# Kernel tuning notes

Measured on AMD Instinct MI355X. Metric: run time of the kernel, lower is better.

## Reference

```python
import jax, jax.numpy as jnp
import numpy as np

E = 16        # ensemble size
D_IN = 512    # input_dim
H = 512       # hidden width (hidden=[512,512])
D_OUT = 1     # output_dim
B = 8192      # batch


def _xavier(key, shape, fan_in, fan_out):
    # Xavier/Glorot uniform, matching layer_init='Xavier'
    limit = np.sqrt(6.0 / (fan_in + fan_out)).astype(np.float32)
    return jax.random.uniform(key, shape, jnp.float32, -limit, limit)


def setup_inputs() -> dict:
    key = jax.random.key(0)
    ks = jax.random.split(key, 7)
    x = jax.random.normal(ks[0], (B, D_IN), dtype=jnp.float32)
    # stacked per-ensemble-member weights (equivalent to E independent MLPs)
    W1 = _xavier(ks[1], (E, D_IN, H), D_IN, H)
    b1 = jnp.zeros((E, H), dtype=jnp.float32)
    W2 = _xavier(ks[2], (E, H, H), H, H)
    b2 = jnp.zeros((E, H), dtype=jnp.float32)
    W3 = _xavier(ks[3], (E, H, D_OUT), H, D_OUT)
    b3 = jnp.zeros((E, D_OUT), dtype=jnp.float32)
    return {"x": x, "W1": W1, "b1": b1, "W2": W2, "b2": b2, "W3": W3, "b3": b3}


def reference(x, W1, b1, W2, b2, W3, b3):
    # Batched over the ensemble dim: one grouped GEMM per layer instead of E small ones.
    h1 = jax.nn.relu(jnp.einsum('bi,eih->ebh', x, W1) + b1[:, None, :])   # [E,B,H]
    h2 = jax.nn.relu(jnp.einsum('ebh,ehk->ebk', h1, W2) + b2[:, None, :])  # [E,B,H]
    out = jnp.einsum('ebh,eho->ebo', h2, W3) + b3[:, None, :]              # [E,B,D_OUT]
    return out
```

## Files before the change

kernel.cpp:

```cpp
#include <hip/hip_runtime.h>


#define E_N   16
#define DIN   512
#define HID   512
#define BATCH 8192
#define BT    64
#define NBT   (BATCH / BT)
#define NBLK  (E_N * NBT)

typedef __attribute__((ext_vector_type(8))) short bf16x8;
typedef __attribute__((ext_vector_type(4))) float f32x4;

#define IMG_BYTES   131072
#define XPACK_BYTES ((size_t)NBT * IMG_BYTES)
#define WP_PER_E    (32 * 16 * 2048)
#define WP_BYTES    ((size_t)E_N * WP_PER_E)

__device__ __forceinline__ short f2bf(float f) {
  unsigned u = __builtin_bit_cast(unsigned, f);
  u += 0x7fffu + ((u >> 16) & 1u);
  return (short)(u >> 16);
}
__device__ __forceinline__ float bf2f(short s) {
  unsigned u = ((unsigned)(unsigned short)s) << 16;
  return __builtin_bit_cast(float, u);
}

__global__ void pack_x_kernel(const float* __restrict__ x, char* __restrict__ xp) {
  int t  = blockIdx.x * blockDim.x + threadIdx.x;
  int b  = t >> 6;
  int c8 = (t & 63) << 3;
  const float* src = x + (size_t)b * DIN + c8;
  bf16x8 hi, lo;
#pragma unroll
  for (int j = 0; j < 8; ++j) {
    float v = src[j];
    short h = f2bf(v);
    hi[j] = h;
    lo[j] = f2bf(v - bf2f(h));
  }
  int btile = b >> 6, r = b & 63;
  char* img = xp + (size_t)btile * IMG_BYTES;
  int inrow = (c8 << 1) ^ ((r & 7) << 4);
  *(bf16x8*)(img + (r << 10) + inrow) = hi;
  *(bf16x8*)(img + 65536 + (r << 10) + inrow) = lo;
}

__global__ void pack_w_kernel(const float* __restrict__ w, char* __restrict__ wp) {
  int t    = blockIdx.x * blockDim.x + threadIdx.x;
  int lane = t & 63;
  int kb   = (t >> 6) & 15;
  int nt   = (t >> 10) & 31;
  int e    = t >> 15;
  int k0 = kb * 32 + (lane >> 4) * 8;
  int n  = nt * 16 + (lane & 15);
  const float* src = w + ((size_t)e * DIN + k0) * HID + n;
  bf16x8 hi, lo;
#pragma unroll
  for (int j = 0; j < 8; ++j) {
    float v = src[(size_t)j * HID];
    short h = f2bf(v);
    hi[j] = h;
    lo[j] = f2bf(v - bf2f(h));
  }
  char* dst = wp + ((size_t)((e * 32 + nt) * 16 + kb) << 11) + (lane << 4);
  *(bf16x8*)dst = hi;
  *(bf16x8*)(dst + 1024) = lo;
}

#define MFMA(A, B, C) __builtin_amdgcn_mfma_f32_16x16x32_bf16(A, B, C, 0, 0, 0)

__global__ __launch_bounds__(512, 2) void fused_mlp_kernel(
    const char* __restrict__ xp,
    const char* __restrict__ wp1,
    const char* __restrict__ wp2,
    const float* __restrict__ b1,
    const float* __restrict__ b2,
    const float* __restrict__ w3,
    const float* __restrict__ b3,
    float* __restrict__ out)
{
  __shared__ __align__(16) char lds[IMG_BYTES];
  __shared__ float out_acc[BT];

  const int tid  = threadIdx.x;
  const int lane = tid & 63;
  const int wid  = tid >> 6;

  const int bid   = blockIdx.x;
  const int xcd   = bid & 7;
  const int slot  = bid >> 3;
  const int e     = (xcd << 1) | (slot >> 7);
  const int btile = slot & 127;

  {
    const char* src = xp + (size_t)btile * IMG_BYTES;
#pragma unroll
    for (int it = 0; it < 16; ++it) {
      int off = (it << 13) + (tid << 4);
      *(bf16x8*)(lds + off) = *(const bf16x8*)(src + off);
    }
  }
  if (tid < BT) out_acc[tid] = b3[e];

  const int swzA = (lane & 7) << 4;
  const int h4   = (lane >> 4) << 4;
  int rb[4];
#pragma unroll
  for (int mt = 0; mt < 4; ++mt) rb[mt] = (mt * 16 + (lane & 15)) << 10;

  float bias1[4], bias2[4], w3v[4];
#pragma unroll
  for (int ntl = 0; ntl < 4; ++ntl) {
    int c = wid * 64 + ntl * 16 + (lane & 15);
    bias1[ntl] = b1[e * HID + c];
    bias2[ntl] = b2[e * HID + c];
    w3v[ntl]   = w3[e * HID + c];
  }

  const char* wpe1 = wp1 + (size_t)e * WP_PER_E + (size_t)wid * (4 * 16 * 2048);
  const char* wpe2 = wp2 + (size_t)e * WP_PER_E + (size_t)wid * (4 * 16 * 2048);

  __syncthreads();

  f32x4 acc[4][4];
#pragma unroll
  for (int mt = 0; mt < 4; ++mt)
#pragma unroll
    for (int ntl = 0; ntl < 4; ++ntl)
      acc[mt][ntl] = (f32x4){0.f, 0.f, 0.f, 0.f};

#pragma unroll 4
  for (int kb = 0; kb < 16; ++kb) {
    bf16x8 Ah[4], Al[4], Bh[4], Bl[4];
    const int ca = ((kb << 6) | h4) ^ swzA;
#pragma unroll
    for (int mt = 0; mt < 4; ++mt) {
      Ah[mt] = *(const bf16x8*)(lds + rb[mt] + ca);
      Al[mt] = *(const bf16x8*)(lds + 65536 + rb[mt] + ca);
    }
#pragma unroll
    for (int ntl = 0; ntl < 4; ++ntl) {
      const char* p = wpe1 + ((ntl * 16 + kb) << 11) + (lane << 4);
      Bh[ntl] = *(const bf16x8*)p;
      Bl[ntl] = *(const bf16x8*)(p + 1024);
    }
#pragma unroll
    for (int mt = 0; mt < 4; ++mt)
#pragma unroll
      for (int ntl = 0; ntl < 4; ++ntl) {
        acc[mt][ntl] = MFMA(Ah[mt], Bh[ntl], acc[mt][ntl]);
        acc[mt][ntl] = MFMA(Ah[mt], Bl[ntl], acc[mt][ntl]);
        acc[mt][ntl] = MFMA(Al[mt], Bh[ntl], acc[mt][ntl]);
      }
  }

  __syncthreads();

#pragma unroll
  for (int mt = 0; mt < 4; ++mt)
#pragma unroll
    for (int ntl = 0; ntl < 4; ++ntl) {
      const int C2 = (wid * 64 + ntl * 16 + (lane & 15)) << 1;
#pragma unroll
      for (int q = 0; q < 4; ++q) {
        const int R = mt * 16 + (lane >> 4) * 4 + q;
        float v = acc[mt][ntl][q] + bias1[ntl];
        v = fmaxf(v, 0.f);
        short hb = f2bf(v);
        short lb = f2bf(v - bf2f(hb));
        const int inrow = C2 ^ ((R & 7) << 4);
        *(short*)(lds + (R << 10) + inrow) = hb;
        *(short*)(lds + 65536 + (R << 10) + inrow) = lb;
      }
    }

  __syncthreads();

#pragma unroll
  for (int mt = 0; mt < 4; ++mt)
#pragma unroll
    for (int ntl = 0; ntl < 4; ++ntl)
      acc[mt][ntl] = (f32x4){0.f, 0.f, 0.f, 0.f};

#pragma unroll 4
  for (int kb = 0; kb < 16; ++kb) {
    bf16x8 Ah[4], Al[4], Bh[4], Bl[4];
    const int ca = ((kb << 6) | h4) ^ swzA;
#pragma unroll
    for (int mt = 0; mt < 4; ++mt) {
      Ah[mt] = *(const bf16x8*)(lds + rb[mt] + ca);
      Al[mt] = *(const bf16x8*)(lds + 65536 + rb[mt] + ca);
    }
#pragma unroll
    for (int ntl = 0; ntl < 4; ++ntl) {
      const char* p = wpe2 + ((ntl * 16 + kb) << 11) + (lane << 4);
      Bh[ntl] = *(const bf16x8*)p;
      Bl[ntl] = *(const bf16x8*)(p + 1024);
    }
#pragma unroll
    for (int mt = 0; mt < 4; ++mt)
#pragma unroll
      for (int ntl = 0; ntl < 4; ++ntl) {
        acc[mt][ntl] = MFMA(Ah[mt], Bh[ntl], acc[mt][ntl]);
        acc[mt][ntl] = MFMA(Ah[mt], Bl[ntl], acc[mt][ntl]);
        acc[mt][ntl] = MFMA(Al[mt], Bh[ntl], acc[mt][ntl]);
      }
  }

#pragma unroll
  for (int mt = 0; mt < 4; ++mt)
#pragma unroll
    for (int q = 0; q < 4; ++q) {
      float p = 0.f;
#pragma unroll
      for (int ntl = 0; ntl < 4; ++ntl)
        p += fmaxf(acc[mt][ntl][q] + bias2[ntl], 0.f) * w3v[ntl];
      p += __shfl_xor(p, 1);
      p += __shfl_xor(p, 2);
      p += __shfl_xor(p, 4);
      p += __shfl_xor(p, 8);
      if ((lane & 15) == 0)
        atomicAdd(&out_acc[mt * 16 + (lane >> 4) * 4 + q], p);
    }

  __syncthreads();
  if (tid < BT)
    out[(size_t)e * BATCH + btile * BT + tid] = out_acc[tid];
}

extern "C" void kernel_launch(void* const* d_in, const int* in_sizes, int n_in,
                              void* d_out, int out_size, void* d_ws, size_t ws_size,
                              hipStream_t stream) {
  (void)in_sizes; (void)n_in; (void)out_size; (void)ws_size;
  const float* x  = (const float*)d_in[0];
  const float* W1 = (const float*)d_in[1];
  const float* b1 = (const float*)d_in[2];
  const float* W2 = (const float*)d_in[3];
  const float* b2 = (const float*)d_in[4];
  const float* W3 = (const float*)d_in[5];
  const float* b3 = (const float*)d_in[6];

  char* xp  = (char*)d_ws;
  char* wp1 = xp + XPACK_BYTES;
  char* wp2 = wp1 + WP_BYTES;

  pack_x_kernel<<<2048, 256, 0, stream>>>(x, xp);
  pack_w_kernel<<<2048, 256, 0, stream>>>(W1, wp1);
  pack_w_kernel<<<2048, 256, 0, stream>>>(W2, wp2);
  fused_mlp_kernel<<<NBLK, 512, 0, stream>>>(xp, wp1, wp2, b1, b2, W3, b3,
                                             (float*)d_out);
}
```

Measured before the change: 438.3 us.

## Switch GEMMs to 32x32x16 MFMA with repacked weights and prefetched B fragments

Replaces the 16x16x32 bf16 MFMA tiling with 32x32x16 MFMA tiles (2x2 per wave), and repacks the weights and the x image with a 16-row XOR swizzle to match the new fragment layout. B fragments for the next k-block are double-buffered in registers so the global loads overlap the current MFMAs. The larger MFMA shape is meant to lower LDS A-fragment reads per flop and raise matrix-core efficiency. In exchange, register pressure rises from the prefetch buffers and 16-wide accumulators, which could hurt occupancy at the 2-blocks launch bound.

After: 492.8 us. 12.4% more time.

```diff
diff --git a/kernel.cpp b/kernel.cpp
--- a/kernel.cpp
+++ b/kernel.cpp
@@ -10,11 +10,11 @@
 #define NBLK  (E_N * NBT)
 
 typedef __attribute__((ext_vector_type(8))) short bf16x8;
-typedef __attribute__((ext_vector_type(4))) float f32x4;
+typedef __attribute__((ext_vector_type(16))) float f32x16;
 
 #define IMG_BYTES   131072
 #define XPACK_BYTES ((size_t)NBT * IMG_BYTES)
-#define WP_PER_E    (32 * 16 * 2048)
+#define WP_PER_E    (1 << 20)
 #define WP_BYTES    ((size_t)E_N * WP_PER_E)
 
 __device__ __forceinline__ short f2bf(float f) {
@@ -42,7 +42,7 @@
   }
   int btile = b >> 6, r = b & 63;
   char* img = xp + (size_t)btile * IMG_BYTES;
-  int inrow = (c8 << 1) ^ ((r & 7) << 4);
+  int inrow = (c8 << 1) ^ ((r & 15) << 4);
   *(bf16x8*)(img + (r << 10) + inrow) = hi;
   *(bf16x8*)(img + 65536 + (r << 10) + inrow) = lo;
 }
@@ -50,11 +50,12 @@
 __global__ void pack_w_kernel(const float* __restrict__ w, char* __restrict__ wp) {
   int t    = blockIdx.x * blockDim.x + threadIdx.x;
   int lane = t & 63;
-  int kb   = (t >> 6) & 15;
-  int nt   = (t >> 10) & 31;
+  int kk   = (t >> 6) & 1;
+  int kb   = (t >> 7) & 15;
+  int nt   = (t >> 11) & 15;
   int e    = t >> 15;
-  int k0 = kb * 32 + (lane >> 4) * 8;
-  int n  = nt * 16 + (lane & 15);
+  int k0 = kb * 32 + kk * 16 + (lane >> 5) * 8;
+  int n  = nt * 32 + (lane & 31);
   const float* src = w + ((size_t)e * DIN + k0) * HID + n;
   bf16x8 hi, lo;
 #pragma unroll
@@ -64,12 +65,24 @@
     hi[j] = h;
     lo[j] = f2bf(v - bf2f(h));
   }
-  char* dst = wp + ((size_t)((e * 32 + nt) * 16 + kb) << 11) + (lane << 4);
+  char* dst = wp + (((size_t)(e * 16 + nt) * 16 + kb) << 12) + (kk << 11) + (lane << 4);
   *(bf16x8*)dst = hi;
   *(bf16x8*)(dst + 1024) = lo;
 }
 
-#define MFMA(A, B, C) __builtin_amdgcn_mfma_f32_16x16x32_bf16(A, B, C, 0, 0, 0)
+#define MFMA32(A, B, C) __builtin_amdgcn_mfma_f32_32x32x16_bf16(A, B, C, 0, 0, 0)
+
+#define LOADB(dst, kb_) do {                                          \
+    const int _k = (kb_) << 12;                                       \
+    dst[0] = *(const bf16x8*)(w0 + _k);                               \
+    dst[1] = *(const bf16x8*)(w0 + _k + 1024);                        \
+    dst[2] = *(const bf16x8*)(w0 + _k + 2048);                        \
+    dst[3] = *(const bf16x8*)(w0 + _k + 3072);                        \
+    dst[4] = *(const bf16x8*)(w1 + _k);                               \
+    dst[5] = *(const bf16x8*)(w1 + _k + 1024);                        \
+    dst[6] = *(const bf16x8*)(w1 + _k + 2048);                        \
+    dst[7] = *(const bf16x8*)(w1 + _k + 3072);                        \
+  } while (0)
 
 __global__ __launch_bounds__(512, 2) void fused_mlp_kernel(
     const char* __restrict__ xp,
@@ -84,9 +97,12 @@
   __shared__ __align__(16) char lds[IMG_BYTES];
   __shared__ float out_acc[BT];
 
-  const int tid  = threadIdx.x;
-  const int lane = tid & 63;
-  const int wid  = tid >> 6;
+  const int tid    = threadIdx.x;
+  const int lane   = tid & 63;
+  const int wid    = tid >> 6;
+  const int lane31 = lane & 31;
+  const int hk16   = (lane >> 5) << 4;
+  const int aswz   = (lane & 15) << 4;
 
   const int bid   = blockIdx.x;
   const int xcd   = bid & 7;
@@ -104,73 +120,81 @@
   }
   if (tid < BT) out_acc[tid] = b3[e];
 
-  const int swzA = (lane & 7) << 4;
-  const int h4   = (lane >> 4) << 4;
-  int rb[4];
-#pragma unroll
-  for (int mt = 0; mt < 4; ++mt) rb[mt] = (mt * 16 + (lane & 15)) << 10;
-
-  float bias1[4], bias2[4], w3v[4];
-#pragma unroll
-  for (int ntl = 0; ntl < 4; ++ntl) {
-    int c = wid * 64 + ntl * 16 + (lane & 15);
+  int arow[2];
+#pragma unroll
+  for (int mt = 0; mt < 2; ++mt) arow[mt] = ((mt << 5) + lane31) << 10;
+
+  float bias1[2], bias2[2], w3v[2];
+#pragma unroll
+  for (int ntl = 0; ntl < 2; ++ntl) {
+    int c = wid * 64 + ntl * 32 + lane31;
     bias1[ntl] = b1[e * HID + c];
     bias2[ntl] = b2[e * HID + c];
     w3v[ntl]   = w3[e * HID + c];
   }
 
-  const char* wpe1 = wp1 + (size_t)e * WP_PER_E + (size_t)wid * (4 * 16 * 2048);
-  const char* wpe2 = wp2 + (size_t)e * WP_PER_E + (size_t)wid * (4 * 16 * 2048);
-
-  __syncthreads();
-
-  f32x4 acc[4][4];
-#pragma unroll
-  for (int mt = 0; mt < 4; ++mt)
-#pragma unroll
-    for (int ntl = 0; ntl < 4; ++ntl)
-      acc[mt][ntl] = (f32x4){0.f, 0.f, 0.f, 0.f};
-
-#pragma unroll 4
-  for (int kb = 0; kb < 16; ++kb) {
-    bf16x8 Ah[4], Al[4], Bh[4], Bl[4];
-    const int ca = ((kb << 6) | h4) ^ swzA;
-#pragma unroll
-    for (int mt = 0; mt < 4; ++mt) {
-      Ah[mt] = *(const bf16x8*)(lds + rb[mt] + ca);
-      Al[mt] = *(const bf16x8*)(lds + 65536 + rb[mt] + ca);
-    }
-#pragma unroll
-    for (int ntl = 0; ntl < 4; ++ntl) {
-      const char* p = wpe1 + ((ntl * 16 + kb) << 11) + (lane << 4);
-      Bh[ntl] = *(const bf16x8*)p;
-      Bl[ntl] = *(const bf16x8*)(p + 1024);
-    }
-#pragma unroll
-    for (int mt = 0; mt < 4; ++mt)
-#pragma unroll
-      for (int ntl = 0; ntl < 4; ++ntl) {
-        acc[mt][ntl] = MFMA(Ah[mt], Bh[ntl], acc[mt][ntl]);
-        acc[mt][ntl] = MFMA(Ah[mt], Bl[ntl], acc[mt][ntl]);
-        acc[mt][ntl] = MFMA(Al[mt], Bh[ntl], acc[mt][ntl]);
-      }
-  }
-
-  __syncthreads();
-
-#pragma unroll
-  for (int mt = 0; mt < 4; ++mt)
-#pragma unroll
-    for (int ntl = 0; ntl < 4; ++ntl) {
-      const int C2 = (wid * 64 + ntl * 16 + (lane & 15)) << 1;
-#pragma unroll
-      for (int q = 0; q < 4; ++q) {
-        const int R = mt * 16 + (lane >> 4) * 4 + q;
-        float v = acc[mt][ntl][q] + bias1[ntl];
+  const char* wA0 = wp1 + (size_t)e * WP_PER_E + ((size_t)(wid * 2 + 0) << 16) + (lane << 4);
+  const char* wA1 = wp1 + (size_t)e * WP_PER_E + ((size_t)(wid * 2 + 1) << 16) + (lane << 4);
+  const char* wB0 = wp2 + (size_t)e * WP_PER_E + ((size_t)(wid * 2 + 0) << 16) + (lane << 4);
+  const char* wB1 = wp2 + (size_t)e * WP_PER_E + ((size_t)(wid * 2 + 1) << 16) + (lane << 4);
+
+  __syncthreads();
+
+  f32x16 acc[2][2];
+
+  auto run_layer = [&](const char* w0, const char* w1) {
+    bf16x8 Bb[2][8];
+    LOADB(Bb[0], 0);
+#pragma unroll
+    for (int kb = 0; kb < 16; ++kb) {
+      if (kb < 15) LOADB(Bb[(kb + 1) & 1], kb + 1);
+      bf16x8 Ah[2][2], Al[2][2];
+#pragma unroll
+      for (int mt = 0; mt < 2; ++mt)
+#pragma unroll
+        for (int kk = 0; kk < 2; ++kk) {
+          const int off = ((kb << 6) + (kk << 5) + hk16) ^ aswz;
+          const char* pa = lds + arow[mt] + off;
+          Ah[mt][kk] = *(const bf16x8*)pa;
+          Al[mt][kk] = *(const bf16x8*)(pa + 65536);
+        }
+#pragma unroll
+      for (int mt = 0; mt < 2; ++mt)
+#pragma unroll
+        for (int ntl = 0; ntl < 2; ++ntl)
+#pragma unroll
+          for (int kk = 0; kk < 2; ++kk) {
+            const int fb = ntl * 4 + kk * 2;
+            acc[mt][ntl] = MFMA32(Ah[mt][kk], Bb[kb & 1][fb],     acc[mt][ntl]);
+            acc[mt][ntl] = MFMA32(Ah[mt][kk], Bb[kb & 1][fb + 1], acc[mt][ntl]);
+            acc[mt][ntl] = MFMA32(Al[mt][kk], Bb[kb & 1][fb],     acc[mt][ntl]);
+          }
+    }
+  };
+
+#pragma unroll
+  for (int mt = 0; mt < 2; ++mt)
+#pragma unroll
+    for (int ntl = 0; ntl < 2; ++ntl)
+      acc[mt][ntl] = (f32x16)(0.f);
+
+  run_layer(wA0, wA1);
+
+  __syncthreads();
+
+#pragma unroll
+  for (int mt = 0; mt < 2; ++mt)
+#pragma unroll
+    for (int ntl = 0; ntl < 2; ++ntl) {
+      const int C2 = (wid * 64 + ntl * 32 + lane31) << 1;
+#pragma unroll
+      for (int reg = 0; reg < 16; ++reg) {
+        const int R = mt * 32 + (reg & 3) + 8 * (reg >> 2) + ((lane >> 5) << 2);
+        float v = acc[mt][ntl][reg] + bias1[ntl];
         v = fmaxf(v, 0.f);
         short hb = f2bf(v);
         short lb = f2bf(v - bf2f(hb));
-        const int inrow = C2 ^ ((R & 7) << 4);
+        const int inrow = C2 ^ ((R & 15) << 4);
         *(short*)(lds + (R << 10) + inrow) = hb;
         *(short*)(lds + 65536 + (R << 10) + inrow) = lb;
       }
@@ -179,50 +203,30 @@
   __syncthreads();
 
 #pragma unroll
-  for (int mt = 0; mt < 4; ++mt)
-#pragma unroll
-    for (int ntl = 0; ntl < 4; ++ntl)
-      acc[mt][ntl] = (f32x4){0.f, 0.f, 0.f, 0.f};
-
-#pragma unroll 4
-  for (int kb = 0; kb < 16; ++kb) {
-    bf16x8 Ah[4], Al[4], Bh[4], Bl[4];
-    const int ca = ((kb << 6) | h4) ^ swzA;
-#pragma unroll
-    for (int mt = 0; mt < 4; ++mt) {
-      Ah[mt] = *(const bf16x8*)(lds + rb[mt] + ca);
-      Al[mt] = *(const bf16x8*)(lds + 65536 + rb[mt] + ca);
-    }
-#pragma unroll
-    for (int ntl = 0; ntl < 4; ++ntl) {
-      const char* p = wpe2 + ((ntl * 16 + kb) << 11) + (lane << 4);
-      Bh[ntl] = *(const bf16x8*)p;
-      Bl[ntl] = *(const bf16x8*)(p + 1024);
-    }
-#pragma unroll
-    for (int mt = 0; mt < 4; ++mt)
-#pragma unroll
-      for (int ntl = 0; ntl < 4; ++ntl) {
-        acc[mt][ntl] = MFMA(Ah[mt], Bh[ntl], acc[mt][ntl]);
-        acc[mt][ntl] = MFMA(Ah[mt], Bl[ntl], acc[mt][ntl]);
-        acc[mt][ntl] = MFMA(Al[mt], Bh[ntl], acc[mt][ntl]);
-      }
-  }
-
-#pragma unroll
-  for (int mt = 0; mt < 4; ++mt)
-#pragma unroll
-    for (int q = 0; q < 4; ++q) {
+  for (int mt = 0; mt < 2; ++mt)
+#pragma unroll
+    for (int ntl = 0; ntl < 2; ++ntl)
+      acc[mt][ntl] = (f32x16)(0.f);
+
+  run_layer(wB0, wB1);
+
+#pragma unroll
+  for (int mt = 0; mt < 2; ++mt)
+#pragma unroll
+    for (int reg = 0; reg < 16; ++reg) {
       float p = 0.f;
 #pragma unroll
-      for (int ntl = 0; ntl < 4; ++ntl)
-        p += fmaxf(acc[mt][ntl][q] + bias2[ntl], 0.f) * w3v[ntl];
+      for (int ntl = 0; ntl < 2; ++ntl)
+        p += fmaxf(acc[mt][ntl][reg] + bias2[ntl], 0.f) * w3v[ntl];
       p += __shfl_xor(p, 1);
       p += __shfl_xor(p, 2);
       p += __shfl_xor(p, 4);
       p += __shfl_xor(p, 8);
-      if ((lane & 15) == 0)
-        atomicAdd(&out_acc[mt * 16 + (lane >> 4) * 4 + q], p);
+      p += __shfl_xor(p, 16);
+      if (lane31 == 0) {
+        const int R = mt * 32 + (reg & 3) + 8 * (reg >> 2) + ((lane >> 5) << 2);
+        atomicAdd(&out_acc[R], p);
+      }
     }
 
   __syncthreads();
```

## Split fused MLP across 16 waves with prefetched B fragments and wider swizzle

Applied to the files above, without the earlier changes.

Doubles the block to 1024 threads so each of 16 waves computes a 64x32 output slice instead of 64x64, raising wave-level parallelism per CU. Weight fragments are software double-buffered across k-steps to hide global load latency behind MFMAs. The LDS XOR swizzle is widened from 8 to 16 rows in both the pack and epilogue writes to cut bank conflicts. In exchange, A fragments are re-read from LDS twice as often per MFMA, and the aggressive launch bounds may constrain registers and cause spills.

Measured after the change: 480.4 us. 9.6% more time.

```diff
diff --git a/kernel.cpp b/kernel.cpp
--- a/kernel.cpp
+++ b/kernel.cpp
@@ -42,7 +42,7 @@
   }
   int btile = b >> 6, r = b & 63;
   char* img = xp + (size_t)btile * IMG_BYTES;
-  int inrow = (c8 << 1) ^ ((r & 7) << 4);
+  int inrow = (c8 << 1) ^ ((r & 15) << 4);
   *(bf16x8*)(img + (r << 10) + inrow) = hi;
   *(bf16x8*)(img + 65536 + (r << 10) + inrow) = lo;
 }
@@ -69,9 +69,17 @@
   *(bf16x8*)(dst + 1024) = lo;
 }
 
-#define MFMA(A, B, C) __builtin_amdgcn_mfma_f32_16x16x32_bf16(A, B, C, 0, 0, 0)
-
-__global__ __launch_bounds__(512, 2) void fused_mlp_kernel(
+#define MFMA16(A, B, C) __builtin_amdgcn_mfma_f32_16x16x32_bf16(A, B, C, 0, 0, 0)
+
+#define LOADB(dst, kb_) do {                                          \
+    const int _k = (kb_) << 11;                                       \
+    dst[0] = *(const bf16x8*)(w0 + _k);                               \
+    dst[1] = *(const bf16x8*)(w0 + _k + 1024);                        \
+    dst[2] = *(const bf16x8*)(w1 + _k);                               \
+    dst[3] = *(const bf16x8*)(w1 + _k + 1024);                        \
+  } while (0)
+
+__global__ __launch_bounds__(1024, 4) void fused_mlp_kernel(
     const char* __restrict__ xp,
     const char* __restrict__ wp1,
     const char* __restrict__ wp2,
@@ -84,9 +92,12 @@
   __shared__ __align__(16) char lds[IMG_BYTES];
   __shared__ float out_acc[BT];
 
-  const int tid  = threadIdx.x;
-  const int lane = tid & 63;
-  const int wid  = tid >> 6;
+  const int tid    = threadIdx.x;
+  const int lane   = tid & 63;
+  const int wid    = tid >> 6;
+  const int lane15 = lane & 15;
+  const int h4     = (lane >> 4) << 4;
+  const int aswz   = lane15 << 4;
 
   const int bid   = blockIdx.x;
   const int xcd   = bid & 7;
@@ -97,72 +108,77 @@
   {
     const char* src = xp + (size_t)btile * IMG_BYTES;
 #pragma unroll
-    for (int it = 0; it < 16; ++it) {
-      int off = (it << 13) + (tid << 4);
+    for (int it = 0; it < 8; ++it) {
+      int off = (it << 14) + (tid << 4);
       *(bf16x8*)(lds + off) = *(const bf16x8*)(src + off);
     }
   }
   if (tid < BT) out_acc[tid] = b3[e];
 
-  const int swzA = (lane & 7) << 4;
-  const int h4   = (lane >> 4) << 4;
   int rb[4];
 #pragma unroll
-  for (int mt = 0; mt < 4; ++mt) rb[mt] = (mt * 16 + (lane & 15)) << 10;
-
-  float bias1[4], bias2[4], w3v[4];
-#pragma unroll
-  for (int ntl = 0; ntl < 4; ++ntl) {
-    int c = wid * 64 + ntl * 16 + (lane & 15);
+  for (int mt = 0; mt < 4; ++mt) rb[mt] = ((mt << 4) + lane15) << 10;
+
+  float bias1[2], bias2[2], w3v[2];
+#pragma unroll
+  for (int ntl = 0; ntl < 2; ++ntl) {
+    int c = wid * 32 + ntl * 16 + lane15;
     bias1[ntl] = b1[e * HID + c];
     bias2[ntl] = b2[e * HID + c];
     w3v[ntl]   = w3[e * HID + c];
   }
 
-  const char* wpe1 = wp1 + (size_t)e * WP_PER_E + (size_t)wid * (4 * 16 * 2048);
-  const char* wpe2 = wp2 + (size_t)e * WP_PER_E + (size_t)wid * (4 * 16 * 2048);
-
-  __syncthreads();
-
-  f32x4 acc[4][4];
-#pragma unroll
-  for (int mt = 0; mt < 4; ++mt)
-#pragma unroll
-    for (int ntl = 0; ntl < 4; ++ntl)
+  const char* wA0 = wp1 + (size_t)e * WP_PER_E + ((size_t)(wid * 2 + 0) << 15) + (lane << 4);
+  const char* wA1 = wp1 + (size_t)e * WP_PER_E + ((size_t)(wid * 2 + 1) << 15) + (lane << 4);
+  const char* wB0 = wp2 + (size_t)e * WP_PER_E + ((size_t)(wid * 2 + 0) << 15) + (lane << 4);
+  const char* wB1 = wp2 + (size_t)e * WP_PER_E + ((size_t)(wid * 2 + 1) << 15) + (lane << 4);
+
+  __syncthreads();
+
+  f32x4 acc[4][2];
+
+  auto run_layer = [&](const char* w0, const char* w1) {
+    bf16x8 Bb[2][4];
+    LOADB(Bb[0], 0);
+#pragma unroll
+    for (int kb = 0; kb < 16; ++kb) {
+      if (kb < 15) LOADB(Bb[(kb + 1) & 1], kb + 1);
+      bf16x8 Ah[4], Al[4];
+      const int ca = ((kb << 6) + h4) ^ aswz;
+#pragma unroll
+      for (int mt = 0; mt < 4; ++mt) {
+        const char* pa = lds + rb[mt] + ca;
+        Ah[mt] = *(const bf16x8*)pa;
+        Al[mt] = *(const bf16x8*)(pa + 65536);
+      }
+#pragma unroll
+      for (int mt = 0; mt < 4; ++mt)
+#pragma unroll
+        for (int ntl = 0; ntl < 2; ++ntl) {
+          const bf16x8 bh = Bb[kb & 1][ntl * 2];
+          const bf16x8 bl = Bb[kb & 1][ntl * 2 + 1];
+          acc[mt][ntl] = MFMA16(Ah[mt], bh, acc[mt][ntl]);
+          acc[mt][ntl] = MFMA16(Ah[mt], bl, acc[mt][ntl]);
+          acc[mt][ntl] = MFMA16(Al[mt], bh, acc[mt][ntl]);
+        }
+    }
+  };
+
+#pragma unroll
+  for (int mt = 0; mt < 4; ++mt)
+#pragma unroll
+    for (int ntl = 0; ntl < 2; ++ntl)
       acc[mt][ntl] = (f32x4){0.f, 0.f, 0.f, 0.f};
 
-#pragma unroll 4
-  for (int kb = 0; kb < 16; ++kb) {
-    bf16x8 Ah[4], Al[4], Bh[4], Bl[4];
-    const int ca = ((kb << 6) | h4) ^ swzA;
-#pragma unroll
-    for (int mt = 0; mt < 4; ++mt) {
-      Ah[mt] = *(const bf16x8*)(lds + rb[mt] + ca);
-      Al[mt] = *(const bf16x8*)(lds + 65536 + rb[mt] + ca);
-    }
-#pragma unroll
-    for (int ntl = 0; ntl < 4; ++ntl) {
-      const char* p = wpe1 + ((ntl * 16 + kb) << 11) + (lane << 4);
-      Bh[ntl] = *(const bf16x8*)p;
-      Bl[ntl] = *(const bf16x8*)(p + 1024);
-    }
-#pragma unroll
-    for (int mt = 0; mt < 4; ++mt)
-#pragma unroll
-      for (int ntl = 0; ntl < 4; ++ntl) {
-        acc[mt][ntl] = MFMA(Ah[mt], Bh[ntl], acc[mt][ntl]);
-        acc[mt][ntl] = MFMA(Ah[mt], Bl[ntl], acc[mt][ntl]);
-        acc[mt][ntl] = MFMA(Al[mt], Bh[ntl], acc[mt][ntl]);
-      }
-  }
-
-  __syncthreads();
-
-#pragma unroll
-  for (int mt = 0; mt < 4; ++mt)
-#pragma unroll
-    for (int ntl = 0; ntl < 4; ++ntl) {
-      const int C2 = (wid * 64 + ntl * 16 + (lane & 15)) << 1;
+  run_layer(wA0, wA1);
+
+  __syncthreads();
+
+#pragma unroll
+  for (int mt = 0; mt < 4; ++mt)
+#pragma unroll
+    for (int ntl = 0; ntl < 2; ++ntl) {
+      const int C2 = (wid * 32 + ntl * 16 + lane15) << 1;
 #pragma unroll
       for (int q = 0; q < 4; ++q) {
         const int R = mt * 16 + (lane >> 4) * 4 + q;
@@ -170,7 +186,7 @@
         v = fmaxf(v, 0.f);
         short hb = f2bf(v);
         short lb = f2bf(v - bf2f(hb));
-        const int inrow = C2 ^ ((R & 7) << 4);
+        const int inrow = C2 ^ ((R & 15) << 4);
         *(short*)(lds + (R << 10) + inrow) = hb;
         *(short*)(lds + 65536 + (R << 10) + inrow) = lb;
       }
@@ -181,33 +197,10 @@
 #pragma unroll
   for (int mt = 0; mt < 4; ++mt)
 #pragma unroll
-    for (int ntl = 0; ntl < 4; ++ntl)
+    for (int ntl = 0; ntl < 2; ++ntl)
       acc[mt][ntl] = (f32x4){0.f, 0.f, 0.f, 0.f};
 
-#pragma unroll 4
-  for (int kb = 0; kb < 16; ++kb) {
-    bf16x8 Ah[4], Al[4], Bh[4], Bl[4];
-    const int ca = ((kb << 6) | h4) ^ swzA;
-#pragma unroll
-    for (int mt = 0; mt < 4; ++mt) {
-      Ah[mt] = *(const bf16x8*)(lds + rb[mt] + ca);
-      Al[mt] = *(const bf16x8*)(lds + 65536 + rb[mt] + ca);
-    }
-#pragma unroll
-    for (int ntl = 0; ntl < 4; ++ntl) {
-      const char* p = wpe2 + ((ntl * 16 + kb) << 11) + (lane << 4);
-      Bh[ntl] = *(const bf16x8*)p;
-      Bl[ntl] = *(const bf16x8*)(p + 1024);
-    }
-#pragma unroll
-    for (int mt = 0; mt < 4; ++mt)
-#pragma unroll
-      for (int ntl = 0; ntl < 4; ++ntl) {
-        acc[mt][ntl] = MFMA(Ah[mt], Bh[ntl], acc[mt][ntl]);
-        acc[mt][ntl] = MFMA(Ah[mt], Bl[ntl], acc[mt][ntl]);
-        acc[mt][ntl] = MFMA(Al[mt], Bh[ntl], acc[mt][ntl]);
-      }
-  }
+  run_layer(wB0, wB1);
 
 #pragma unroll
   for (int mt = 0; mt < 4; ++mt)
@@ -215,13 +208,13 @@
     for (int q = 0; q < 4; ++q) {
       float p = 0.f;
 #pragma unroll
-      for (int ntl = 0; ntl < 4; ++ntl)
+      for (int ntl = 0; ntl < 2; ++ntl)
         p += fmaxf(acc[mt][ntl][q] + bias2[ntl], 0.f) * w3v[ntl];
       p += __shfl_xor(p, 1);
       p += __shfl_xor(p, 2);
       p += __shfl_xor(p, 4);
       p += __shfl_xor(p, 8);
-      if ((lane & 15) == 0)
+      if (lane15 == 0)
         atomicAdd(&out_acc[mt * 16 + (lane >> 4) * 4 + q], p);
     }
 
@@ -249,6 +242,6 @@
   pack_x_kernel<<<2048, 256, 0, stream>>>(x, xp);
   pack_w_kernel<<<2048, 256, 0, stream>>>(W1, wp1);
   pack_w_kernel<<<2048, 256, 0, stream>>>(W2, wp2);
-  fused_mlp_kernel<<<NBLK, 512, 0, stream>>>(xp, wp1, wp2, b1, b2, W3, b3,
-                                             (float*)d_out);
-}
+  fused_mlp_kernel<<<NBLK, 1024, 0, stream>>>(xp, wp1, wp2, b1, b2, W3, b3,
+                                              (float*)d_out);
+}
```
